# Kernel optimization log

Hardware: AMD Instinct MI355X
Metric: run time of the kernel (lower is better)

The kernel has to match this reference:

```python
import jax, jax.numpy as jnp
import numpy as np

B = 2048    # graphs in batch
V = 15      # nodes per graph
T = 16      # window (args.n_his)
F_IN = 2    # num_features
H = 64      # nhid
LH = 40     # LSTM hidden per direction
EPER = 40   # edges per graph
N = B * V
E = B * EPER
EPS = 1e-5


def setup_inputs() -> dict:
    key = jax.random.key(0)
    ks = jax.random.split(key, 12)

    def rn(k, shape, fan_in):
        return jax.random.normal(k, shape, jnp.float32) / np.sqrt(fan_in).astype(np.float32)

    # block-diagonal batched edge_index (PyG-style batching of B graphs of V nodes)
    rng = np.random.default_rng(0)
    off = np.arange(B)[:, None] * V
    src = rng.integers(0, V, (B, EPER)) + off
    dst = rng.integers(0, V, (B, EPER)) + off
    edge_index = jnp.asarray(np.stack([src.ravel(), dst.ravel()]), dtype=jnp.int32)

    return {
        "data": jax.random.normal(ks[0], (N, F_IN, T), jnp.float32),
        "edge_attr": jax.random.uniform(ks[1], (E,), jnp.float32),
        "W1": rn(ks[2], (H, F_IN), F_IN), "b1": jnp.zeros((H,), jnp.float32),
        "Wg1": rn(ks[3], (H, H), H), "bg1": jnp.zeros((H,), jnp.float32),
        "gamma1": jnp.ones((H,), jnp.float32), "beta1": jnp.zeros((H,), jnp.float32),
        "Wg2": rn(ks[4], (H, H), H), "bg2": jnp.zeros((H,), jnp.float32),
        "gamma2": jnp.ones((H,), jnp.float32), "beta2": jnp.zeros((H,), jnp.float32),
        "Wf": rn(ks[5], (H, V * H), V * H), "bf": jnp.zeros((H,), jnp.float32),
        "Wih_f": rn(ks[6], (4 * LH, H), H), "Whh_f": rn(ks[7], (4 * LH, LH), LH),
        "bih_f": jnp.zeros((4 * LH,), jnp.float32), "bhh_f": jnp.zeros((4 * LH,), jnp.float32),
        "Wih_b": rn(ks[8], (4 * LH, H), H), "Whh_b": rn(ks[9], (4 * LH, LH), LH),
        "bih_b": jnp.zeros((4 * LH,), jnp.float32), "bhh_b": jnp.zeros((4 * LH,), jnp.float32),
        "Wc1": rn(ks[10], (16, 2 * LH), 2 * LH), "bc1": jnp.zeros((16,), jnp.float32),
        "Wc2": rn(ks[11], (1, 16), 16), "bc2": jnp.zeros((1,), jnp.float32),
        "edge_index": edge_index,
    }


def _gcn(x, W, b, edge_index, ew):
    # PyG GCNConv: linear, add self-loops (weight 1), symmetric D^-1/2 (A+I) D^-1/2.
    # x: [N, T, H] -- all T timesteps processed at once (vectorizes the source loop).
    row, col = edge_index[0], edge_index[1]
    loop = jnp.arange(N, dtype=edge_index.dtype)
    row_s = jnp.concatenate([row, loop])
    col_s = jnp.concatenate([col, loop])
    ew_s = jnp.concatenate([ew, jnp.ones((N,), ew.dtype)])
    deg = jax.ops.segment_sum(ew_s, col_s, num_segments=N)
    dinv = jnp.where(deg > 0, jax.lax.rsqrt(deg), 0.0)
    norm = dinv[row_s] * ew_s * dinv[col_s]                      # [E+N]
    xw = jnp.einsum('nth,hk->ntk', x, W)                          # [N, T, H]
    agg = jax.ops.segment_sum(norm[:, None, None] * xw[row_s], col_s, num_segments=N)
    return agg + b


def _bn(x, gamma, beta):
    # BatchNorm1d training-mode stats, per timestep (axis 0 = nodes), biased var.
    m = x.mean(axis=0)
    v = x.var(axis=0)
    return gamma * (x - m) * jax.lax.rsqrt(v + EPS) + beta


def _lstm(X, Wih, Whh, bih, bhh):
    # X: [T, B, H]; PyTorch gate order i, f, g, o.
    def step(carry, xt):
        h, c = carry
        g = xt @ Wih.T + h @ Whh.T + (bih + bhh)
        i, f, gg, o = jnp.split(g, 4, axis=-1)
        c = jax.nn.sigmoid(f) * c + jax.nn.sigmoid(i) * jnp.tanh(gg)
        h = jax.nn.sigmoid(o) * jnp.tanh(c)
        return (h, c), h
    h0 = jnp.zeros((X.shape[1], LH), X.dtype)
    _, hs = jax.lax.scan(step, (h0, h0), X)
    return hs


def _forward(data, edge_attr, W1, b1, Wg1, bg1, gamma1, beta1, Wg2, bg2, gamma2, beta2,
             Wf, bf, Wih_f, Whh_f, bih_f, bhh_f, Wih_b, Whh_b, bih_b, bhh_b,
             Wc1, bc1, Wc2, bc2, edge_index):
    # conv_1 (1x1 Conv2d) == per-node linear over features, kept per timestep
    x = jnp.einsum('nft,hf->nth', data, W1) + b1                 # [N, T, H]
    # Hierarchical GCN with residuals (ReLU then BN, per the source)
    x1 = _bn(jax.nn.relu(_gcn(x, Wg1, bg1, edge_index, edge_attr)), gamma1, beta1) + x
    x2 = _bn(jax.nn.relu(_gcn(x1, Wg2, bg2, edge_index, edge_attr)), gamma2, beta2) + x1
    # stack over timesteps -> [T, B, V*H]
    Xs = x2.transpose(1, 0, 2).reshape(T, B, V * H)
    Xs = jax.nn.relu(Xs @ Wf.T + bf)                             # fc1 -> [T, B, H]
    hs_f = _lstm(Xs, Wih_f, Whh_f, bih_f, bhh_f)
    hs_b = _lstm(Xs[::-1], Wih_b, Whh_b, bih_b, bhh_b)
    # r_out[-1] = [fwd h at t=T-1, bwd h at t=T-1 (first step of reversed scan)]
    last = jnp.concatenate([hs_f[-1], hs_b[0]], axis=-1)          # [B, 80]
    hcls = jax.nn.relu(last @ Wc1.T + bc1)                        # dropout inactive (eval)
    return hcls @ Wc2.T + bc2                                     # [B, 1]


def reference(data, edge_attr, W1, b1, Wg1, bg1, gamma1, beta1, Wg2, bg2, gamma2, beta2,
              Wf, bf, Wih_f, Whh_f, bih_f, bhh_f, Wih_b, Whh_b, bih_b, bhh_b,
              Wc1, bc1, Wc2, bc2, edge_index):
    return _forward(data, edge_attr, W1, b1, Wg1, bg1, gamma1, beta1, Wg2, bg2,
                    gamma2, beta2, Wf, bf, Wih_f, Whh_f, bih_f, bhh_f,
                    Wih_b, Whh_b, bih_b, bhh_b, Wc1, bc1, Wc2, bc2, edge_index)
```

## Files before the change

kernel.cpp:

```cpp
#include <hip/hip_runtime.h>

typedef unsigned int u32;
typedef unsigned short u16;
typedef __attribute__((ext_vector_type(8))) short bf16x8;
typedef __attribute__((ext_vector_type(4))) float f32x4;

#define NB   2048
#define NV   15
#define NT   16
#define NH   64
#define NLH  40
#define EPER 40
#define NN   (NB*NV)
#define NE   (NB*EPER)

#define F_DATA 0
#define F_EA   983040
#define P_W1   1064960
#define P_B1   1065088
#define P_WG1  1065152
#define P_BG1  1069248
#define P_G1   1069312
#define P_BE1  1069376
#define P_WG2  1069440
#define P_BG2  1073536
#define P_G2   1073600
#define P_BE2  1073664
#define P_WF   1073728
#define P_BF   1135168
#define P_WIHF 1135232
#define P_WHHF 1145472
#define P_BIHF 1151872
#define P_BHHF 1152032
#define P_WIHB 1152192
#define P_WHHB 1162432
#define P_BIHB 1168832
#define P_BHHB 1168992
#define P_WC1  1169152
#define P_BC1  1170432
#define P_WC2  1170448
#define P_BC2  1170464
#define CVT_TOTAL 1170465
#define WFB_OFF   1170496
#define WIHT_OFF  1205504
#define STATS_OFF 1231936
#define XS_OFF    1240128
#define FLAG_OFF  3337280
#define BUFX_BYTE 13349376
#define BUFY_BYTE 76263936

#define FR_TOTAL (CVT_TOTAL + 90112 + 4096)

__device__ const int d_cum[27] = {
  0, 983040, 1064960, 1065088, 1065152, 1069248, 1069312, 1069376,
  1069440, 1073536, 1073600, 1073664, 1073728, 1135168, 1135232, 1145472,
  1151872, 1152032, 1152192, 1162432, 1168832, 1168992, 1169152, 1170432,
  1170448, 1170464, 1170465};

struct Ptrs { const void* p[26]; };

__device__ inline float b2f(u16 u) { return __uint_as_float(((u32)u) << 16); }
__device__ inline u16 f2b(float f) {
  u32 u = __float_as_uint(f);
  u32 r = (u + 0x7FFFu + ((u >> 16) & 1u)) >> 16;
  return (u16)r;
}
__device__ inline float sigf(float x) { return 1.0f / (1.0f + __expf(-x)); }
__device__ inline float cvt(const void* src, int j, int flag) {
  return flag ? b2f(((const u16*)src)[j]) : ((const float*)src)[j];
}

__global__ void k_frontend(Ptrs ptrs, float* __restrict__ W) {
  __shared__ int s_flag;
  if (threadIdx.x == 0) s_flag = 1;
  __syncthreads();
  {
    float f = b2f(((const u16*)ptrs.p[0])[threadIdx.x]);
    if (!(fabsf(f) < 1000.0f)) atomicAnd(&s_flag, 0);
  }
  __syncthreads();
  int flag = s_flag;
  int gid = blockIdx.x * 256 + threadIdx.x;
  if (gid == 0) *(int*)(W + FLAG_OFF) = flag;
  if (gid < CVT_TOTAL) {
    int ti = 0;
    #pragma unroll
    for (int i = 1; i < 26; ++i) ti += (gid >= d_cum[i]);
    W[gid] = cvt(ptrs.p[ti], gid - d_cum[ti], flag);
  } else if (gid < CVT_TOTAL + 61440) {
    int i = gid - CVT_TOTAL;
    int j = i & 7, lane = (i >> 3) & 63, kt = (i >> 9) & 3, ks = i >> 11;
    int kout = kt * 16 + (lane & 15);
    int m = ks * 32 + ((lane >> 4) << 3) + j;
    ((u16*)(W + WFB_OFF))[i] = f2b(cvt(ptrs.p[12], kout * 960 + m, flag));
  } else if (gid < CVT_TOTAL + 69632) {
    int ii = gid - CVT_TOTAL - 61440;
    int L = ii >> 12, r = ii & 4095;
    int j = r & 7, lane = (r >> 3) & 63, nt = (r >> 9) & 3, ks = (r >> 11) & 1;
    int h = ks * 32 + ((lane >> 4) << 3) + j;
    int k = nt * 16 + (lane & 15);
    ((u16*)(W + WFB_OFF))[61440 + ii] = f2b(cvt(ptrs.p[L ? 8 : 4], h * 64 + k, flag));
  } else if (gid < CVT_TOTAL + 90112) {
    int e = gid - CVT_TOTAL - 69632;
    int which = e / 10240, rem = e % 10240;
    int kk = rem / 160, jj = rem % 160;
    W[WIHT_OFF + e] = cvt(ptrs.p[which ? 18 : 14], jj * 64 + kk, flag);
  } else if (gid < FR_TOTAL) {
    W[STATS_OFF + (gid - CVT_TOTAL - 90112)] = 0.f;
  }
}

__global__ void k_buildM(const float* __restrict__ W, const int* __restrict__ ei,
                         float* __restrict__ Mout) {
  __shared__ float s_m[960];
  __shared__ float s_deg[64];
  int tid = threadIdx.x;
  int gl = tid >> 6, sub = tid & 63;
  int g = blockIdx.x * 4 + gl;
  float* m = s_m + gl * 240;
  float* deg = s_deg + gl * 16;
  float ew = 0.f; int er = 0, ec = 0;
  if (sub < 40) {
    er = ei[g * 40 + sub] - g * 15;
    ec = ei[NE + g * 40 + sub] - g * 15;
    ew = W[F_EA + g * 40 + sub];
  }
  if (sub >= 40 && sub < 56) deg[sub - 40] = 1.0f;
  #pragma unroll
  for (int c = 0; c < 4; ++c) { int i = sub + c * 64; if (i < 240) m[i] = 0.f; }
  __syncthreads();
  if (sub < 40) atomicAdd(&deg[ec], ew);
  __syncthreads();
  if (sub < 15) deg[sub] = rsqrtf(deg[sub]);
  __syncthreads();
  if (sub < 40) atomicAdd(&m[ec * 16 + er], deg[er] * ew * deg[ec]);
  if (sub >= 40 && sub < 55) {
    float dv = deg[sub - 40];
    atomicAdd(&m[(sub - 40) * 17], dv * dv);
  }
  __syncthreads();
  #pragma unroll
  for (int c = 0; c < 4; ++c) { int i = sub + c * 64; if (i < 240) Mout[g * 240 + i] = m[i]; }
}

template<int LAYER>
__global__ __launch_bounds__(256, 4)
void k_gcn(const float* __restrict__ W, const float* __restrict__ Mg,
           const u16* __restrict__ bufIn, u16* __restrict__ bufOut,
           const u16* __restrict__ WgB,
           float* __restrict__ S1, float* __restrict__ S2,
           int bgoff, int scoff, int shoff) {
  __shared__ u16 s_x[15360];
  __shared__ float s_m[240];
  __shared__ float s_d[480];
  __shared__ float s_w1[192];

  int g = blockIdx.x, tid = threadIdx.x;

  uint4 ld[8];
  if (LAYER == 2) {
    const uint4* py = (const uint4*)(bufIn + g * 15360);
    #pragma unroll
    for (int c = 0; c < 7; ++c) ld[c] = py[tid + c * 256];
    if (tid < 128) ld[7] = py[tid + 1792];
  }

  if (tid < 60) ((float4*)s_m)[tid] = ((const float4*)(Mg + g * 240))[tid];
  if (tid >= 64 && tid < 184) ((float4*)s_d)[tid - 64] = ((const float4*)(W + F_DATA + g * 480))[tid - 64];
  if (tid >= 192 && tid < 240) ((float4*)s_w1)[tid - 192] = ((const float4*)(W + P_W1))[tid - 192];
  __syncthreads();

  #pragma unroll
  for (int c = 0; c < 8; ++c) {
    if (c < 7 || tid < 128) {
      int i = tid + c * 256;
      int v = i >> 7, rem = i & 127, t = rem >> 3, q = rem & 7;
      int h0 = q * 8;
      float d0 = s_d[v * 32 + t], d1 = s_d[v * 32 + 16 + t];
      u32 pk[4];
      if (LAYER == 1) {
        #pragma unroll
        for (int jp = 0; jp < 4; ++jp) {
          int h = h0 + jp * 2;
          float xa = fmaf(d0, s_w1[2 * h],     fmaf(d1, s_w1[2 * h + 1], s_w1[128 + h]));
          float xb = fmaf(d0, s_w1[2 * h + 2], fmaf(d1, s_w1[2 * h + 3], s_w1[129 + h]));
          pk[jp] = (u32)f2b(xa) | ((u32)f2b(xb) << 16);
        }
      } else {
        u32 uys[4] = {ld[c].x, ld[c].y, ld[c].z, ld[c].w};
        int th0 = t * 64 + h0;
        float4 A0 = *(const float4*)(W + scoff + th0), A1 = *(const float4*)(W + scoff + th0 + 4);
        float4 B0 = *(const float4*)(W + shoff + th0), B1 = *(const float4*)(W + shoff + th0 + 4);
        float scs[8] = {A0.x, A0.y, A0.z, A0.w, A1.x, A1.y, A1.z, A1.w};
        float shs[8] = {B0.x, B0.y, B0.z, B0.w, B1.x, B1.y, B1.z, B1.w};
        #pragma unroll
        for (int jp = 0; jp < 4; ++jp) {
          int j0 = jp * 2, h = h0 + j0;
          float xa = fmaf(d0, s_w1[2 * h],     fmaf(d1, s_w1[2 * h + 1], s_w1[128 + h]));
          float xb = fmaf(d0, s_w1[2 * h + 2], fmaf(d1, s_w1[2 * h + 3], s_w1[129 + h]));
          float a = fmaf(b2f((u16)(uys[jp] & 0xffff)), scs[j0],     shs[j0])     + xa;
          float b = fmaf(b2f((u16)(uys[jp] >> 16)),    scs[j0 + 1], shs[j0 + 1]) + xb;
          pk[jp] = (u32)f2b(a) | ((u32)f2b(b) << 16);
        }
      }
      u32 byte = ((u32)(i * 16)) ^ (((u32)(t & 7)) << 4);
      *(uint4*)((char*)s_x + byte) = make_uint4(pk[0], pk[1], pk[2], pk[3]);
    }
  }
  __syncthreads();

  u32* sx32 = (u32*)s_x;
  {
    float x0[15], x1[15], x2[15], x3[15];
    int p0 = tid, p1 = tid + 256;
    int t0 = p0 >> 5, h0 = (2 * p0) & 63;
    int t1 = p1 >> 5, h1 = (2 * p1) & 63;
    u32 ba0 = ((u32)(t0 * 128 + h0 * 2)) ^ (((u32)(t0 & 7)) << 4);
    u32 ba1 = ((u32)(t1 * 128 + h1 * 2)) ^ (((u32)(t1 & 7)) << 4);
    #pragma unroll
    for (int v = 0; v < 15; ++v) {
      u32 ua = sx32[(ba0 + v * 2048) >> 2];
      u32 ub = sx32[(ba1 + v * 2048) >> 2];
      x0[v] = b2f((u16)(ua & 0xffff)); x1[v] = b2f((u16)(ua >> 16));
      x2[v] = b2f((u16)(ub & 0xffff)); x3[v] = b2f((u16)(ub >> 16));
    }
    #pragma unroll
    for (int vc = 0; vc < 15; ++vc) {
      float a0 = 0.f, a1 = 0.f, a2 = 0.f, a3 = 0.f;
      #pragma unroll
      for (int vr = 0; vr < 15; ++vr) {
        float m = s_m[vc * 16 + vr];
        a0 = fmaf(m, x0[vr], a0); a1 = fmaf(m, x1[vr], a1);
        a2 = fmaf(m, x2[vr], a2); a3 = fmaf(m, x3[vr], a3);
      }
      sx32[(ba0 + vc * 2048) >> 2] = (u32)f2b(a0) | ((u32)f2b(a1) << 16);
      sx32[(ba1 + vc * 2048) >> 2] = (u32)f2b(a2) | ((u32)f2b(a3) << 16);
    }
  }
  __syncthreads();

  int wid = tid >> 6, lane = tid & 63;
  int tA = lane & 15, kg = lane >> 4;
  const bf16x8* wb = (const bf16x8*)WgB;
  bf16x8 bf0 = wb[(0 * 4 + wid) * 64 + lane];
  bf16x8 bf1 = wb[(1 * 4 + wid) * 64 + lane];
  int kout = wid * 16 + tA;
  float bias = W[bgoff + kout];
  f32x4 acc[15];
  #pragma unroll
  for (int v = 0; v < 15; ++v) acc[v] = (f32x4){0.f, 0.f, 0.f, 0.f};
  u32 sw = ((u32)(tA & 7)) << 4;
  #pragma unroll
  for (int v = 0; v < 15; ++v) {
    u32 bb = (u32)(v * 2048 + tA * 128 + kg * 16);
    bf16x8 a0 = *(const bf16x8*)(s_x + ((bb ^ sw) >> 1));
    bf16x8 a1 = *(const bf16x8*)(s_x + (((bb + 64) ^ sw) >> 1));
    acc[v] = __builtin_amdgcn_mfma_f32_16x16x32_bf16(a0, bf0, acc[v], 0, 0, 0);
    acc[v] = __builtin_amdgcn_mfma_f32_16x16x32_bf16(a1, bf1, acc[v], 0, 0, 0);
  }

  float s1r[4] = {0.f, 0.f, 0.f, 0.f}, s2r[4] = {0.f, 0.f, 0.f, 0.f};
  __syncthreads();
  #pragma unroll
  for (int v = 0; v < 15; ++v) {
    #pragma unroll
    for (int r = 0; r < 4; ++r) {
      float y = fmaxf(acc[v][r] + bias, 0.f);
      int t = kg * 4 + r;
      u32 byte = ((u32)(v * 2048 + t * 128 + kout * 2)) ^ (((u32)kg) << 5);
      *(u16*)((char*)s_x + byte) = f2b(y);
      s1r[r] += y; s2r[r] += y * y;
    }
  }
  __syncthreads();
  uint4* dst = (uint4*)(bufOut + g * 15360);
  const uint4* src = (const uint4*)s_x;
  #pragma unroll
  for (int c = 0; c < 8; ++c) {
    if (c < 7 || tid < 128) {
      int i = tid + c * 256;
      dst[i] = src[i ^ (((i >> 5) & 3) << 1)];
    }
  }
  #pragma unroll
  for (int r = 0; r < 4; ++r) {
    int idx = (kg * 4 + r) * 64 + kout;
    atomicAdd(&S1[idx], s1r[r]);
    atomicAdd(&S2[idx], s2r[r]);
  }
}

__global__ void k_finalize(float* __restrict__ W, int layer) {
  int i = blockIdx.x * 256 + threadIdx.x;
  if (i >= 1024) return;
  int base = STATS_OFF + (layer == 1 ? 0 : 2048);
  int scb  = STATS_OFF + (layer == 1 ? 4096 : 6144);
  float m   = W[base + i] * (1.0f / 30720.0f);
  float var = W[base + 1024 + i] * (1.0f / 30720.0f) - m * m;
  float istd = rsqrtf(var + 1e-5f);
  int h = i & 63;
  float gm = W[(layer == 1 ? P_G1 : P_G2) + h];
  float bt = W[(layer == 1 ? P_BE1 : P_BE2) + h];
  float sc = gm * istd;
  W[scb + i] = sc;
  W[scb + 1024 + i] = bt - m * sc;
}

__global__ __launch_bounds__(256, 4)
void k_fc1(const float* __restrict__ W, const u16* __restrict__ bufY2,
           const u16* __restrict__ bufY1, const u16* __restrict__ WfB,
           float* __restrict__ Xs) {
  __shared__ u16 s_x[15360];
  __shared__ float s_d[480];
  __shared__ float s_w1[192];
  int g = blockIdx.x, tid = threadIdx.x;
  if (tid < 120) ((float4*)s_d)[tid] = ((const float4*)(W + F_DATA + g * 480))[tid];
  if (tid >= 128 && tid < 176) ((float4*)s_w1)[tid - 128] = ((const float4*)(W + P_W1))[tid - 128];
  __syncthreads();
  const uint4* py2 = (const uint4*)(bufY2 + g * 15360);
  const uint4* py1 = (const uint4*)(bufY1 + g * 15360);
  #pragma unroll
  for (int c = 0; c < 8; ++c) {
    if (c < 7 || tid < 128) {
      int i = tid + c * 256;
      int v = i >> 7, rem = i & 127, t = rem >> 3, q = rem & 7;
      int h0 = q * 8, th0 = t * 64 + h0;
      uint4 u2 = py2[i], u1 = py1[i];
      u32 u2s[4] = {u2.x, u2.y, u2.z, u2.w}, u1s[4] = {u1.x, u1.y, u1.z, u1.w};
      float d0 = s_d[v * 32 + t], d1 = s_d[v * 32 + 16 + t];
      float4 A0 = *(const float4*)(W + STATS_OFF + 6144 + th0), A1 = *(const float4*)(W + STATS_OFF + 6148 + th0);
      float4 B0 = *(const float4*)(W + STATS_OFF + 7168 + th0), B1 = *(const float4*)(W + STATS_OFF + 7172 + th0);
      float4 C0 = *(const float4*)(W + STATS_OFF + 4096 + th0), C1 = *(const float4*)(W + STATS_OFF + 4100 + th0);
      float4 D0 = *(const float4*)(W + STATS_OFF + 5120 + th0), D1 = *(const float4*)(W + STATS_OFF + 5124 + th0);
      float sc2[8] = {A0.x, A0.y, A0.z, A0.w, A1.x, A1.y, A1.z, A1.w};
      float sh2[8] = {B0.x, B0.y, B0.z, B0.w, B1.x, B1.y, B1.z, B1.w};
      float sc1[8] = {C0.x, C0.y, C0.z, C0.w, C1.x, C1.y, C1.z, C1.w};
      float sh1[8] = {D0.x, D0.y, D0.z, D0.w, D1.x, D1.y, D1.z, D1.w};
      u32 pk[4];
      #pragma unroll
      for (int jp = 0; jp < 4; ++jp) {
        int j0 = jp * 2, h = h0 + j0;
        float xa = fmaf(d0, s_w1[2 * h],     fmaf(d1, s_w1[2 * h + 1], s_w1[128 + h]));
        float xb = fmaf(d0, s_w1[2 * h + 2], fmaf(d1, s_w1[2 * h + 3], s_w1[129 + h]));
        float x1a = fmaf(b2f((u16)(u1s[jp] & 0xffff)), sc1[j0],     sh1[j0])     + xa;
        float x1b = fmaf(b2f((u16)(u1s[jp] >> 16)),    sc1[j0 + 1], sh1[j0 + 1]) + xb;
        float a = fmaf(b2f((u16)(u2s[jp] & 0xffff)), sc2[j0],     sh2[j0])     + x1a;
        float b = fmaf(b2f((u16)(u2s[jp] >> 16)),    sc2[j0 + 1], sh2[j0 + 1]) + x1b;
        pk[jp] = (u32)f2b(a) | ((u32)f2b(b) << 16);
      }
      u32 byte = ((u32)(i * 16)) ^ (((u32)(t & 7)) << 4);
      *(uint4*)((char*)s_x + byte) = make_uint4(pk[0], pk[1], pk[2], pk[3]);
    }
  }
  __syncthreads();

  int wid = tid >> 6, lane = tid & 63;
  int tA = lane & 15, kg = lane >> 4;
  f32x4 acc = {0.f, 0.f, 0.f, 0.f};
  const bf16x8* wf = (const bf16x8*)WfB;
  #pragma unroll 2
  for (int ks = 0; ks < 30; ++ks) {
    int v = ks >> 1, half = ks & 1;
    u32 byte = (u32)(v * 2048 + tA * 128 + (half * 32 + kg * 8) * 2) ^ (((u32)(tA & 7)) << 4);
    bf16x8 afrag = *(const bf16x8*)(s_x + (byte >> 1));
    bf16x8 bfrag = wf[(ks * 4 + wid) * 64 + lane];
    acc = __builtin_amdgcn_mfma_f32_16x16x32_bf16(afrag, bfrag, acc, 0, 0, 0);
  }
  int kout = wid * 16 + (lane & 15);
  float bias = W[P_BF + kout];
  #pragma unroll
  for (int r = 0; r < 4; ++r) {
    int t = (lane >> 4) * 4 + r;
    Xs[t * 131072 + g * 64 + kout] = fmaxf(acc[r] + bias, 0.0f);
  }
}

__global__ __launch_bounds__(512)
void k_lstm2(const float* __restrict__ W, const float* __restrict__ Xs,
             void* __restrict__ dout, const int* __restrict__ flagp) {
  extern __shared__ float smem[];
  float* s_whh = smem;
  float* s_xs  = smem + 6480;
  float* s_h   = smem + 14672;
  float* s_c   = smem + 14992;
  float* s_hb  = smem + 15312;
  float* s_g   = smem + 15632;
  float* s_cls = smem + 16912;
  int tid = threadIdx.x, r0 = blockIdx.x * 8;

  for (int i = tid; i < 6400; i += 512) {
    int jj = i / 40, kk = i % 40;
    s_whh[kk * 162 + jj] = W[P_WHHF + i];
  }
  #pragma unroll
  for (int c = 0; c < 4; ++c) {
    int i4 = tid + c * 512;
    int i = i4 * 4;
    int t = i >> 9, b = (i >> 6) & 7, k = i & 63;
    ((float4*)s_xs)[i4] = *(const float4*)(Xs + t * 131072 + (r0 + b) * 64 + k);
  }
  if (tid < 320) { s_h[tid] = 0.f; s_c[tid] = 0.f; }
  __syncthreads();

  int r = tid >> 6, l = tid & 63;
  int l2 = (l < 32) ? l + 128 : l;
  float G0[16], G1[16], G2[16];
  {
    float b0 = W[P_BIHF + l]      + W[P_BHHF + l];
    float b1 = W[P_BIHF + l + 64] + W[P_BHHF + l + 64];
    float b2 = W[P_BIHF + l2]     + W[P_BHHF + l2];
    #pragma unroll
    for (int t = 0; t < 16; ++t) { G0[t] = b0; G1[t] = b1; G2[t] = b2; }
    const float* wih = W + WIHT_OFF;
    const float* xr = s_xs + r * 64;
    for (int kk = 0; kk < 64; ++kk) {
      float w0 = wih[kk * 160 + l];
      float w1 = wih[kk * 160 + l + 64];
      float w2 = wih[kk * 160 + l2];
      #pragma unroll
      for (int t = 0; t < 16; ++t) {
        float xv = xr[t * 512 + kk];
        G0[t] = fmaf(xv, w0, G0[t]);
        G1[t] = fmaf(xv, w1, G1[t]);
        G2[t] = fmaf(xv, w2, G2[t]);
      }
    }
  }

  #pragma unroll
  for (int t = 0; t < 16; ++t) {
    float acc0 = G0[t], acc1 = G1[t], acc2 = G2[t];
    const float* hr = s_h + r * 40;
    #pragma unroll 8
    for (int kk = 0; kk < 40; ++kk) {
      float hv = hr[kk];
      acc0 = fmaf(hv, s_whh[kk * 162 + l], acc0);
      acc1 = fmaf(hv, s_whh[kk * 162 + l + 64], acc1);
      acc2 = fmaf(hv, s_whh[kk * 162 + l2], acc2);
    }
    s_g[r * 160 + l] = acc0;
    s_g[r * 160 + l + 64] = acc1;
    if (l < 32) s_g[r * 160 + l2] = acc2;
    __syncthreads();
    if (tid < 320) {
      int row = tid / 40, jj = tid % 40;
      const float* gr = s_g + row * 160;
      float ig = gr[jj], fg = gr[jj + 40], gg = gr[jj + 80], og = gr[jj + 120];
      float c = sigf(fg) * s_c[tid] + sigf(ig) * tanhf(gg);
      s_c[tid] = c;
      s_h[tid] = sigf(og) * tanhf(c);
    }
    __syncthreads();
  }

  if (tid < 320) {
    int row = tid / 40, jj = tid % 40;
    const float* wb = W + WIHT_OFF + 10240;
    float ai = W[P_BIHB + jj]       + W[P_BHHB + jj];
    float ag = W[P_BIHB + jj + 80]  + W[P_BHHB + jj + 80];
    float ao = W[P_BIHB + jj + 120] + W[P_BHHB + jj + 120];
    const float* xr = s_xs + 15 * 512 + row * 64;
    for (int kk = 0; kk < 64; ++kk) {
      float xv = xr[kk];
      ai = fmaf(xv, wb[kk * 160 + jj], ai);
      ag = fmaf(xv, wb[kk * 160 + jj + 80], ag);
      ao = fmaf(xv, wb[kk * 160 + jj + 120], ao);
    }
    float c = sigf(ai) * tanhf(ag);
    s_hb[tid] = sigf(ao) * tanhf(c);
  }
  __syncthreads();

  if (tid < 128) {
    int rr = tid >> 4, jj = tid & 15;
    float a = W[P_BC1 + jj];
    for (int p = 0; p < 40; ++p) a = fmaf(W[P_WC1 + jj * 80 + p],      s_h[rr * 40 + p],  a);
    for (int p = 0; p < 40; ++p) a = fmaf(W[P_WC1 + jj * 80 + 40 + p], s_hb[rr * 40 + p], a);
    s_cls[rr * 16 + jj] = fmaxf(a, 0.0f);
  }
  __syncthreads();
  if (tid < 8) {
    float o = W[P_BC2];
    #pragma unroll
    for (int jj = 0; jj < 16; ++jj) o = fmaf(W[P_WC2 + jj], s_cls[tid * 16 + jj], o);
    if (*flagp) ((u16*)dout)[r0 + tid] = f2b(o);
    else        ((float*)dout)[r0 + tid] = o;
  }
}

extern "C" void kernel_launch(void* const* d_in, const int* in_sizes, int n_in,
                              void* d_out, int out_size, void* d_ws, size_t ws_size,
                              hipStream_t stream) {
  float* W = (float*)d_ws;
  u16* bufX = (u16*)((char*)d_ws + BUFX_BYTE);
  u16* bufY = (u16*)((char*)d_ws + BUFY_BYTE);
  u16* WfB  = (u16*)(W + WFB_OFF);
  float* Mg = W + XS_OFF;
  const int* ei = (const int*)d_in[26];

  (void)hipFuncSetAttribute(reinterpret_cast<const void*>(&k_lstm2),
                            hipFuncAttributeMaxDynamicSharedMemorySize, 68160);

  Ptrs ptrs;
  for (int i = 0; i < 26; ++i) ptrs.p[i] = d_in[i];
  k_frontend<<<(FR_TOTAL + 255) / 256, 256, 0, stream>>>(ptrs, W);
  k_buildM<<<512, 256, 0, stream>>>(W, ei, Mg);
  k_gcn<1><<<NB, 256, 0, stream>>>(W, Mg, nullptr, bufY, WfB + 61440,
      W + STATS_OFF, W + STATS_OFF + 1024, P_BG1, 0, 0);
  k_finalize<<<4, 256, 0, stream>>>(W, 1);
  k_gcn<2><<<NB, 256, 0, stream>>>(W, Mg, bufY, bufX, WfB + 65536,
      W + STATS_OFF + 2048, W + STATS_OFF + 3072, P_BG2,
      STATS_OFF + 4096, STATS_OFF + 5120);
  k_finalize<<<4, 256, 0, stream>>>(W, 2);
  k_fc1<<<NB, 256, 0, stream>>>(W, bufX, bufY, WfB, W + XS_OFF);
  k_lstm2<<<256, 512, 68160, stream>>>(W, W + XS_OFF, d_out, (const int*)(W + FLAG_OFF));
}
```

Baseline: 334.0 us.

## Reassociate GCN aggregation over linear input and stage BN tables in LDS

Uses linearity to push the sparse-adjacency aggregation through the input linear layer and the BN affine transform. Layer 1 aggregates only the two raw feature channels plus a row-sum term, skipping the 15x15 aggregation over 64 channels. Layer 2 aggregates the raw bf16 activations and applies scale, shift and the recomputed residual per output node using row sums. BN scale/shift tables move into shared memory in both k_gcn and k_fc1, and occupancy hints drop from 4 to 3 blocks to make room, which lowers the number of resident waves.

```diff
diff --git a/kernel.cpp b/kernel.cpp
--- a/kernel.cpp
+++ b/kernel.cpp
@@ -144,7 +144,7 @@
 }
 
 template<int LAYER>
-__global__ __launch_bounds__(256, 4)
+__global__ __launch_bounds__(256, 3)
 void k_gcn(const float* __restrict__ W, const float* __restrict__ Mg,
            const u16* __restrict__ bufIn, u16* __restrict__ bufOut,
            const u16* __restrict__ WgB,
@@ -152,8 +152,11 @@
            int bgoff, int scoff, int shoff) {
   __shared__ u16 s_x[15360];
   __shared__ float s_m[240];
+  __shared__ float s_ad[480];
+  __shared__ float s_rs[16];
   __shared__ float s_d[480];
   __shared__ float s_w1[192];
+  __shared__ float s_sc[1024], s_sh[1024];
 
   int g = blockIdx.x, tid = threadIdx.x;
 
@@ -163,81 +166,106 @@
     #pragma unroll
     for (int c = 0; c < 7; ++c) ld[c] = py[tid + c * 256];
     if (tid < 128) ld[7] = py[tid + 1792];
-  }
-
+    ((float4*)s_sc)[tid] = ((const float4*)(W + scoff))[tid];
+    ((float4*)s_sh)[tid] = ((const float4*)(W + shoff))[tid];
+  }
   if (tid < 60) ((float4*)s_m)[tid] = ((const float4*)(Mg + g * 240))[tid];
   if (tid >= 64 && tid < 184) ((float4*)s_d)[tid - 64] = ((const float4*)(W + F_DATA + g * 480))[tid - 64];
   if (tid >= 192 && tid < 240) ((float4*)s_w1)[tid - 192] = ((const float4*)(W + P_W1))[tid - 192];
   __syncthreads();
 
-  #pragma unroll
-  for (int c = 0; c < 8; ++c) {
-    if (c < 7 || tid < 128) {
-      int i = tid + c * 256;
-      int v = i >> 7, rem = i & 127, t = rem >> 3, q = rem & 7;
-      int h0 = q * 8;
-      float d0 = s_d[v * 32 + t], d1 = s_d[v * 32 + 16 + t];
-      u32 pk[4];
-      if (LAYER == 1) {
+  if (tid < 240) {
+    #pragma unroll
+    for (int e2 = 0; e2 < 2; ++e2) {
+      int e = tid * 2 + e2;
+      int vc = e >> 5, c = e & 31;
+      float a = 0.f;
+      #pragma unroll
+      for (int vr = 0; vr < 15; ++vr) a = fmaf(s_m[vc * 16 + vr], s_d[vr * 32 + c], a);
+      s_ad[e] = a;
+    }
+  } else if (tid < 255) {
+    int vc = tid - 240;
+    float a = 0.f;
+    #pragma unroll
+    for (int vr = 0; vr < 15; ++vr) a += s_m[vc * 16 + vr];
+    s_rs[vc] = a;
+  }
+  __syncthreads();
+
+  if (LAYER == 1) {
+    #pragma unroll
+    for (int c = 0; c < 8; ++c) {
+      if (c < 7 || tid < 128) {
+        int i = tid + c * 256;
+        int v = i >> 7, rem = i & 127, t = rem >> 3, q = rem & 7;
+        int h0 = q * 8;
+        float d0 = s_ad[v * 32 + t], d1 = s_ad[v * 32 + 16 + t];
+        float rsv = s_rs[v];
+        u32 pk[4];
         #pragma unroll
         for (int jp = 0; jp < 4; ++jp) {
           int h = h0 + jp * 2;
-          float xa = fmaf(d0, s_w1[2 * h],     fmaf(d1, s_w1[2 * h + 1], s_w1[128 + h]));
-          float xb = fmaf(d0, s_w1[2 * h + 2], fmaf(d1, s_w1[2 * h + 3], s_w1[129 + h]));
+          float xa = fmaf(d0, s_w1[2 * h],     fmaf(d1, s_w1[2 * h + 1], rsv * s_w1[128 + h]));
+          float xb = fmaf(d0, s_w1[2 * h + 2], fmaf(d1, s_w1[2 * h + 3], rsv * s_w1[129 + h]));
           pk[jp] = (u32)f2b(xa) | ((u32)f2b(xb) << 16);
         }
-      } else {
-        u32 uys[4] = {ld[c].x, ld[c].y, ld[c].z, ld[c].w};
-        int th0 = t * 64 + h0;
-        float4 A0 = *(const float4*)(W + scoff + th0), A1 = *(const float4*)(W + scoff + th0 + 4);
-        float4 B0 = *(const float4*)(W + shoff + th0), B1 = *(const float4*)(W + shoff + th0 + 4);
-        float scs[8] = {A0.x, A0.y, A0.z, A0.w, A1.x, A1.y, A1.z, A1.w};
-        float shs[8] = {B0.x, B0.y, B0.z, B0.w, B1.x, B1.y, B1.z, B1.w};
+        u32 byte = ((u32)(i * 16)) ^ (((u32)(t & 7)) << 4);
+        *(uint4*)((char*)s_x + byte) = make_uint4(pk[0], pk[1], pk[2], pk[3]);
+      }
+    }
+  } else {
+    #pragma unroll
+    for (int c = 0; c < 8; ++c) {
+      if (c < 7 || tid < 128) {
+        int i = tid + c * 256;
+        int t = (i >> 3) & 15;
+        u32 byte = ((u32)(i * 16)) ^ (((u32)(t & 7)) << 4);
+        *(uint4*)((char*)s_x + byte) = ld[c];
+      }
+    }
+  }
+  __syncthreads();
+
+  if (LAYER == 2) {
+    u32* sx32 = (u32*)s_x;
+    #pragma unroll 1
+    for (int pp = 0; pp < 2; ++pp) {
+      int p = tid + pp * 256;
+      int t = p >> 5, h = (2 * p) & 63;
+      int th = t * 64 + h;
+      u32 ba = ((u32)(t * 128 + h * 2)) ^ (((u32)(t & 7)) << 4);
+      float y0[15], y1v[15];
+      #pragma unroll
+      for (int v = 0; v < 15; ++v) {
+        u32 u = sx32[(ba + v * 2048) >> 2];
+        y0[v] = b2f((u16)(u & 0xffff)); y1v[v] = b2f((u16)(u >> 16));
+      }
+      float sc0 = s_sc[th], sc1v = s_sc[th + 1];
+      float sh0 = s_sh[th], sh1v = s_sh[th + 1];
+      float w10 = s_w1[2 * h], w11 = s_w1[2 * h + 1];
+      float w10b = s_w1[2 * h + 2], w11b = s_w1[2 * h + 3];
+      float b1a = s_w1[128 + h], b1b = s_w1[129 + h];
+      #pragma unroll
+      for (int vc = 0; vc < 15; ++vc) {
+        float aY0 = 0.f, aY1 = 0.f;
         #pragma unroll
-        for (int jp = 0; jp < 4; ++jp) {
-          int j0 = jp * 2, h = h0 + j0;
-          float xa = fmaf(d0, s_w1[2 * h],     fmaf(d1, s_w1[2 * h + 1], s_w1[128 + h]));
-          float xb = fmaf(d0, s_w1[2 * h + 2], fmaf(d1, s_w1[2 * h + 3], s_w1[129 + h]));
-          float a = fmaf(b2f((u16)(uys[jp] & 0xffff)), scs[j0],     shs[j0])     + xa;
-          float b = fmaf(b2f((u16)(uys[jp] >> 16)),    scs[j0 + 1], shs[j0 + 1]) + xb;
-          pk[jp] = (u32)f2b(a) | ((u32)f2b(b) << 16);
+        for (int vr = 0; vr < 15; ++vr) {
+          float m = s_m[vc * 16 + vr];
+          aY0 = fmaf(m, y0[vr], aY0);
+          aY1 = fmaf(m, y1v[vr], aY1);
         }
+        float rsv = s_rs[vc];
+        float ad0 = s_ad[vc * 32 + t], ad1 = s_ad[vc * 32 + 16 + t];
+        float ax0 = fmaf(ad0, w10,  fmaf(ad1, w11,  rsv * b1a));
+        float ax1 = fmaf(ad0, w10b, fmaf(ad1, w11b, rsv * b1b));
+        float o0 = fmaf(sc0,  aY0, fmaf(rsv, sh0, ax0));
+        float o1 = fmaf(sc1v, aY1, fmaf(rsv, sh1v, ax1));
+        sx32[(ba + vc * 2048) >> 2] = (u32)f2b(o0) | ((u32)f2b(o1) << 16);
       }
-      u32 byte = ((u32)(i * 16)) ^ (((u32)(t & 7)) << 4);
-      *(uint4*)((char*)s_x + byte) = make_uint4(pk[0], pk[1], pk[2], pk[3]);
-    }
-  }
-  __syncthreads();
-
-  u32* sx32 = (u32*)s_x;
-  {
-    float x0[15], x1[15], x2[15], x3[15];
-    int p0 = tid, p1 = tid + 256;
-    int t0 = p0 >> 5, h0 = (2 * p0) & 63;
-    int t1 = p1 >> 5, h1 = (2 * p1) & 63;
-    u32 ba0 = ((u32)(t0 * 128 + h0 * 2)) ^ (((u32)(t0 & 7)) << 4);
-    u32 ba1 = ((u32)(t1 * 128 + h1 * 2)) ^ (((u32)(t1 & 7)) << 4);
-    #pragma unroll
-    for (int v = 0; v < 15; ++v) {
-      u32 ua = sx32[(ba0 + v * 2048) >> 2];
-      u32 ub = sx32[(ba1 + v * 2048) >> 2];
-      x0[v] = b2f((u16)(ua & 0xffff)); x1[v] = b2f((u16)(ua >> 16));
-      x2[v] = b2f((u16)(ub & 0xffff)); x3[v] = b2f((u16)(ub >> 16));
-    }
-    #pragma unroll
-    for (int vc = 0; vc < 15; ++vc) {
-      float a0 = 0.f, a1 = 0.f, a2 = 0.f, a3 = 0.f;
-      #pragma unroll
-      for (int vr = 0; vr < 15; ++vr) {
-        float m = s_m[vc * 16 + vr];
-        a0 = fmaf(m, x0[vr], a0); a1 = fmaf(m, x1[vr], a1);
-        a2 = fmaf(m, x2[vr], a2); a3 = fmaf(m, x3[vr], a3);
-      }
-      sx32[(ba0 + vc * 2048) >> 2] = (u32)f2b(a0) | ((u32)f2b(a1) << 16);
-      sx32[(ba1 + vc * 2048) >> 2] = (u32)f2b(a2) | ((u32)f2b(a3) << 16);
-    }
-  }
-  __syncthreads();
+    }
+    __syncthreads();
+  }
 
   int wid = tid >> 6, lane = tid & 63;
   int tA = lane & 15, kg = lane >> 4;
@@ -306,14 +334,18 @@
   W[scb + 1024 + i] = bt - m * sc;
 }
 
-__global__ __launch_bounds__(256, 4)
+__global__ __launch_bounds__(256, 3)
 void k_fc1(const float* __restrict__ W, const u16* __restrict__ bufY2,
            const u16* __restrict__ bufY1, const u16* __restrict__ WfB,
            float* __restrict__ Xs) {
   __shared__ u16 s_x[15360];
   __shared__ float s_d[480];
   __shared__ float s_w1[192];
+  __shared__ float s_t[4096];
   int g = blockIdx.x, tid = threadIdx.x;
+  #pragma unroll
+  for (int k = 0; k < 4; ++k)
+    ((float4*)s_t)[tid + k * 256] = ((const float4*)(W + STATS_OFF + 4096))[tid + k * 256];
   if (tid < 120) ((float4*)s_d)[tid] = ((const float4*)(W + F_DATA + g * 480))[tid];
   if (tid >= 128 && tid < 176) ((float4*)s_w1)[tid - 128] = ((const float4*)(W + P_W1))[tid - 128];
   __syncthreads();
@@ -328,10 +360,10 @@
       uint4 u2 = py2[i], u1 = py1[i];
       u32 u2s[4] = {u2.x, u2.y, u2.z, u2.w}, u1s[4] = {u1.x, u1.y, u1.z, u1.w};
       float d0 = s_d[v * 32 + t], d1 = s_d[v * 32 + 16 + t];
-      float4 A0 = *(const float4*)(W + STATS_OFF + 6144 + th0), A1 = *(const float4*)(W + STATS_OFF + 6148 + th0);
-      float4 B0 = *(const float4*)(W + STATS_OFF + 7168 + th0), B1 = *(const float4*)(W + STATS_OFF + 7172 + th0);
-      float4 C0 = *(const float4*)(W + STATS_OFF + 4096 + th0), C1 = *(const float4*)(W + STATS_OFF + 4100 + th0);
-      float4 D0 = *(const float4*)(W + STATS_OFF + 5120 + th0), D1 = *(const float4*)(W + STATS_OFF + 5124 + th0);
+      float4 C0 = *(const float4*)(s_t + th0),        C1 = *(const float4*)(s_t + th0 + 4);
+      float4 D0 = *(const float4*)(s_t + 1024 + th0), D1 = *(const float4*)(s_t + 1028 + th0);
+      float4 A0 = *(const float4*)(s_t + 2048 + th0), A1 = *(const float4*)(s_t + 2052 + th0);
+      float4 B0 = *(const float4*)(s_t + 3072 + th0), B1 = *(const float4*)(s_t + 3076 + th0);
       float sc2[8] = {A0.x, A0.y, A0.z, A0.w, A1.x, A1.y, A1.z, A1.w};
       float sh2[8] = {B0.x, B0.y, B0.z, B0.w, B1.x, B1.y, B1.z, B1.w};
       float sc1[8] = {C0.x, C0.y, C0.z, C0.w, C1.x, C1.y, C1.z, C1.w};
```

New measurement: 433.7 us. 29.9% more time.
